# Optimization experiments

Measured on AMD Instinct MI355X. Metric: run time of the kernel, lower is better.

Reference implementation:

```python
import jax, jax.numpy as jnp
import numpy as np

DIM = 256
NUM_RFS = 256
OUT_DIM = 1024
N = 65536
M = 0.001


def setup_inputs() -> dict:
    key = jax.random.key(0)
    k1, k2, k3, k4, k5, k6 = jax.random.split(key, 6)
    x = jax.random.normal(k1, (N, DIM), dtype=jnp.float32)
    input_weights = jax.random.normal(k2, (OUT_DIM, DIM), dtype=jnp.float32)
    b = jax.random.normal(k3, (OUT_DIM,), dtype=jnp.float32)
    # projection matrix: normal(mean=0, std=0.02, size=(num_rfs, dim))
    proj = 0.02 * jax.random.normal(k4, (NUM_RFS, DIM), dtype=jnp.float32)
    # xis are complex points of the random-feature construction; keep small for exp stability
    xis_real = 0.1 * jax.random.normal(k5, (NUM_RFS,), dtype=jnp.float32)
    xis_imag = 0.1 * jax.random.normal(k6, (NUM_RFS,), dtype=jnp.float32)
    return {"x": x, "input_weights": input_weights, "b": b, "proj": proj,
            "xis_real": xis_real, "xis_imag": xis_imag}


def _asym_feats(xw, xis, proj, bias, is_weight):
    """create_asym_feats with a_fun/b_fun = identity, A_fun/B_fun = exp(xi*b).
    xw: (rows, DIM) float; xis: (NUM_RFS,) complex64; proj: (NUM_RFS, DIM) float.
    Returns (rows, NUM_RFS) complex64."""
    ab = xis  # ab_fun is identity -> ab_coeffs = xis
    scale = np.sqrt(1.0 + 4.0 * M).astype(np.float32)
    # renorm_gs[i] = sqrt(1+4M) * ab[i] * gs[i]  -> (NUM_RFS, DIM) complex
    renorm_gs = scale * ab[:, None] * proj.astype(jnp.complex64)
    # dot_products = xw_c @ renorm_gs.T  -> (rows, NUM_RFS) complex
    dot = jnp.einsum('nd,rd->nr', xw.astype(jnp.complex64), renorm_gs)
    sq = jnp.sum(xw * xw, axis=-1)  # (rows,)
    # correction: outer(sq/2, ab*ab) + M*||g_i||^2 (broadcast over rows)
    corr = (sq[:, None] * 0.5) * (ab * ab)[None, :]
    corr = corr + M * jnp.sum(proj * proj, axis=-1)[None, :]
    feats = jnp.exp(dot - corr) * np.float32(1.0 / np.sqrt(NUM_RFS))
    if is_weight:
        # AB_coeffs[j, i] = exp(xis[i] * bias[j])
        AB = jnp.exp(xis[None, :] * bias[:, None].astype(jnp.complex64))
        feats = AB * feats
    return feats


def reference(x, input_weights, b, proj, xis_real, xis_imag):
    xis = (xis_real + 1j * xis_imag).astype(jnp.complex64)
    # normalize=False path: scale weights and bias by dim**-0.25 at init time
    inv4 = np.float32(1.0 / DIM ** 0.25)
    w = input_weights * inv4
    bb = b * inv4
    c = np.float32((1.0 / np.sqrt(2.0)) * (1.0 + 4.0 * M) ** (DIM / 4.0))
    # precomputed weight features (parameter of the module)
    w_plus = _asym_feats(w, xis, proj, bb, is_weight=True)
    w_minus = _asym_feats(w, -xis, proj, bb, is_weight=True)
    weights = c * jnp.concatenate([w_plus, w_minus], axis=-1)  # (OUT_DIM, 2R) complex
    # forward: x scaled by 1/dim (normalize=False)
    xs = x * np.float32(1.0 / DIM)
    f_plus = _asym_feats(xs, xis, proj, bb, is_weight=False)
    f_minus = _asym_feats(xs, -xis, proj, bb, is_weight=False)
    feat = c * jnp.concatenate([f_plus, f_minus], axis=-1)  # (N, 2R) complex
    # (feat @ weights.T).real
    out = jnp.einsum('nr,or->no', feat, weights).real
    return out
```

## Files before the change

kernel.cpp:

```cpp
#include <hip/hip_runtime.h>
#include <cmath>
#include <cstdint>

#define NROWS 65536
#define DIMN  256
#define NRF   256
#define OUTD  1024
#define KDIM  1024
#define MCOEF 0.001f

typedef __bf16 v8bf __attribute__((ext_vector_type(8)));
typedef float  v4f  __attribute__((ext_vector_type(4)));
typedef unsigned short us8 __attribute__((ext_vector_type(8)));

__device__ __forceinline__ unsigned short f2bf(float f) {
  unsigned int u = __float_as_uint(f);
  u += 0x7fffu + ((u >> 16) & 1u);
  return (unsigned short)(u >> 16);
}

__device__ __forceinline__ void async_copy16(const void* g, void* l) {
  __builtin_amdgcn_global_load_lds(
      (const __attribute__((address_space(1))) void*)g,
      (__attribute__((address_space(3))) void*)l, 16, 0, 0);
}

__device__ __forceinline__ int sw_slot(int r, int c) {
  return r * 4 + ((c ^ (r >> 1)) & 3);
}

__global__ __launch_bounds__(64) void prep_rf(
    const float* __restrict__ proj, unsigned short* __restrict__ projbf,
    float* __restrict__ mg2) {
  int i = blockIdx.x;
  int lane = threadIdx.x;
  float4 v = ((const float4*)(proj + (size_t)i * DIMN))[lane];
  ushort4 o;
  o.x = f2bf(v.x); o.y = f2bf(v.y); o.z = f2bf(v.z); o.w = f2bf(v.w);
  ((ushort4*)(projbf + (size_t)i * DIMN))[lane] = o;
  float ss = v.x * v.x + v.y * v.y + v.z * v.z + v.w * v.w;
#pragma unroll
  for (int off = 32; off > 0; off >>= 1) ss += __shfl_down(ss, off, 64);
  if (lane == 0) mg2[i] = MCOEF * ss;
}

__global__ __launch_bounds__(256) void fused_features(
    const float* __restrict__ srcX,
    const float* __restrict__ srcW,
    const float* __restrict__ biasW,
    const float* __restrict__ xr_g, const float* __restrict__ xi_g,
    const float* __restrict__ mg2_g,
    const unsigned short* __restrict__ projbf,
    unsigned short* __restrict__ FX,
    unsigned short* __restrict__ FW,
    float sRx, float sRw, float scaleC) {
  __shared__ __align__(16) unsigned short big[16 * 1024];
  unsigned short* As = big;
  unsigned short* Bs = big + 2048;
  unsigned short* Os = big;
  __shared__ float xr_s[256], xi_s[256], c1_s[256], c2_s[256], mg2_s[256];
  __shared__ float sq_s[64], bias_s[64];

  int t = threadIdx.x;
  int lane = t & 63;
  int w = t >> 6;

  bool isW = blockIdx.x < (OUTD / 64);
  int blockRow = isW ? blockIdx.x * 64 : (blockIdx.x - OUTD / 64) * 64;
  const float* src = isW ? srcW : srcX;
  float scl = isW ? 0.25f : (1.f / DIMN);
  unsigned short* Fout = isW ? FW : FX;
  float sR = isW ? sRw : sRx;
  float sI = isW ? -sRw : sRx;

  {
    float a = xr_g[t], b = xi_g[t];
    xr_s[t] = a; xi_s[t] = b;
    c1_s[t] = a * a - b * b;
    c2_s[t] = 2.f * a * b;
    mg2_s[t] = mg2_g[t];
  }
  if (t < 64) bias_s[t] = isW ? biasW[blockRow + t] * 0.25f : 0.f;

  v4f acc[4][4];
#pragma unroll
  for (int a = 0; a < 4; a++)
#pragma unroll
    for (int b = 0; b < 4; b++)
#pragma unroll
      for (int q = 0; q < 4; q++) acc[a][b][q] = 0.f;

  int arow = t >> 2, sub = t & 3;
  const float* srow = src + (size_t)(blockRow + arow) * DIMN + sub * 8;
  float ss = 0.f;

  for (int kb = 0; kb < DIMN; kb += 32) {
    float4 v0 = *(const float4*)(srow + kb);
    float4 v1 = *(const float4*)(srow + kb + 4);
    v0.x *= scl; v0.y *= scl; v0.z *= scl; v0.w *= scl;
    v1.x *= scl; v1.y *= scl; v1.z *= scl; v1.w *= scl;
    ss += v0.x * v0.x + v0.y * v0.y + v0.z * v0.z + v0.w * v0.w +
          v1.x * v1.x + v1.y * v1.y + v1.z * v1.z + v1.w * v1.w;
    us8 o;
    o[0] = f2bf(v0.x); o[1] = f2bf(v0.y); o[2] = f2bf(v0.z); o[3] = f2bf(v0.w);
    o[4] = f2bf(v1.x); o[5] = f2bf(v1.y); o[6] = f2bf(v1.z); o[7] = f2bf(v1.w);
    *(us8*)&As[sw_slot(arow, sub) * 8] = o;
#pragma unroll
    for (int r = 0; r < 4; r++) {
      int idx = r * 256 + t;
      int row = idx >> 2, kc = ((idx & 3) ^ ((idx >> 3) & 3)) * 8;
      async_copy16(projbf + (size_t)row * DIMN + kb + kc,
                   Bs + (idx & ~63) * 8);
    }
    __syncthreads();
    v8bf af[4], bfv[4];
    int c = lane >> 4;
#pragma unroll
    for (int mi = 0; mi < 4; mi++)
      af[mi] = *(const v8bf*)&As[sw_slot(mi * 16 + (lane & 15), c) * 8];
#pragma unroll
    for (int ni = 0; ni < 4; ni++)
      bfv[ni] = *(const v8bf*)&Bs[sw_slot(w * 64 + ni * 16 + (lane & 15), c) * 8];
#pragma unroll
    for (int mi = 0; mi < 4; mi++)
#pragma unroll
      for (int ni = 0; ni < 4; ni++)
        acc[mi][ni] = __builtin_amdgcn_mfma_f32_16x16x32_bf16(
            af[mi], bfv[ni], acc[mi][ni], 0, 0, 0);
    __syncthreads();
  }

  ss += __shfl_xor(ss, 1, 64);
  ss += __shfl_xor(ss, 2, 64);
  if (sub == 0) sq_s[arow] = ss;

#pragma unroll
  for (int mi = 0; mi < 4; mi++) {
    __syncthreads();
#pragma unroll
    for (int ni = 0; ni < 4; ni++) {
      int i = w * 64 + ni * 16 + (lane & 15);
      float xrv = xr_s[i], xiv = xi_s[i];
      float c1v = c1_s[i], c2v = c2_s[i], mgv = mg2_s[i];
#pragma unroll
      for (int reg = 0; reg < 4; reg++) {
        int rl    = (lane >> 4) * 4 + reg;
        int rglob = mi * 16 + rl;
        float px = acc[mi][ni][reg];
        float tt = scaleC * px + bias_s[rglob];
        float u  = 0.5f * sq_s[rglob];
        float aa = u * c1v + mgv;
        float bb = u * c2v;
        float txr = tt * xrv;
        float txi = tt * xiv;
        float erp = __expf(txr - aa);
        float erm = __expf(-txr - aa);
        float s1, cc1, s2, cc2;
        __sincosf(txi - bb, &s1, &cc1);
        __sincosf(txi + bb, &s2, &cc2);
        ushort4 ov;
        ov.x = f2bf(sR * erp * cc1);
        ov.y = f2bf(sR * erm * cc2);
        ov.z = f2bf(sI * erp * s1);
        ov.w = f2bf(-sI * erm * s2);
        *(ushort4*)&Os[rl * KDIM + 4 * i] = ov;
      }
    }
    __syncthreads();
#pragma unroll
    for (int j = 0; j < 8; j++) {
      int chunk = j * 256 + t;
      int rowo  = chunk >> 7;
      int off   = (chunk & 127) * 8;
      *(us8*)(Fout + (size_t)(blockRow + mi * 16 + rowo) * KDIM + off) =
          *(const us8*)&Os[rowo * KDIM + off];
    }
  }
}

__global__ __launch_bounds__(256) void gemm_bt(
    const unsigned short* __restrict__ A,
    const unsigned short* __restrict__ B,
    float* __restrict__ C) {
  __shared__ __align__(16) unsigned short As[2][128 * 32];
  __shared__ __align__(16) unsigned short Bs[2][128 * 32];
  int t = threadIdx.x;
  int lane = t & 63;
  int w = t >> 6;
  int wm = w >> 1, wn = w & 1;
  int lid = blockIdx.x;
  int slot = lid >> 3;
  size_t bm = (size_t)(((lid & 7) * 64) + (slot >> 3)) * 128;
  size_t bn = (size_t)(slot & 7) * 128;

  v4f acc[4][4];
#pragma unroll
  for (int a = 0; a < 4; a++)
#pragma unroll
    for (int b = 0; b < 4; b++)
#pragma unroll
      for (int q = 0; q < 4; q++) acc[a][b][q] = 0.f;

  auto stage = [&](int buf, int kb) {
#pragma unroll
    for (int r = 0; r < 2; r++) {
      int idx = r * 256 + t;
      int row = idx >> 2, kc = ((idx & 3) ^ ((idx >> 3) & 3)) * 8;
      async_copy16(A + (bm + row) * KDIM + kb + kc, &As[buf][(idx & ~63) * 8]);
      async_copy16(B + (bn + row) * KDIM + kb + kc, &Bs[buf][(idx & ~63) * 8]);
    }
  };

  auto compute_tile = [&](int buf) {
    v8bf af[4], bfv[4];
    int c = lane >> 4;
#pragma unroll
    for (int mi = 0; mi < 4; mi++)
      af[mi] = *(const v8bf*)&As[buf][sw_slot(wm * 64 + mi * 16 + (lane & 15), c) * 8];
#pragma unroll
    for (int ni = 0; ni < 4; ni++)
      bfv[ni] = *(const v8bf*)&Bs[buf][sw_slot(wn * 64 + ni * 16 + (lane & 15), c) * 8];
#pragma unroll
    for (int mi = 0; mi < 4; mi++)
#pragma unroll
      for (int ni = 0; ni < 4; ni++)
        acc[mi][ni] = __builtin_amdgcn_mfma_f32_16x16x32_bf16(
            af[mi], bfv[ni], acc[mi][ni], 0, 0, 0);
  };

  stage(0, 0);
  asm volatile("s_waitcnt vmcnt(0)" ::: "memory");
  __syncthreads();
  int cur = 0;
  for (int kb = 32; kb < KDIM; kb += 32) {
    stage(cur ^ 1, kb);
    compute_tile(cur);
    asm volatile("s_waitcnt vmcnt(0)" ::: "memory");
    __syncthreads();
    cur ^= 1;
  }
  compute_tile(cur);

#pragma unroll
  for (int mi = 0; mi < 4; mi++)
#pragma unroll
    for (int ni = 0; ni < 4; ni++)
#pragma unroll
      for (int reg = 0; reg < 4; reg++) {
        size_t row = bm + wm * 64 + mi * 16 + (lane >> 4) * 4 + reg;
        size_t col = bn + wn * 64 + ni * 16 + (lane & 15);
        C[row * OUTD + col] = acc[mi][ni][reg];
      }
}

extern "C" void kernel_launch(void* const* d_in, const int* in_sizes, int n_in,
                              void* d_out, int out_size, void* d_ws, size_t ws_size,
                              hipStream_t stream) {
  (void)in_sizes; (void)n_in; (void)out_size;
  const float* x    = (const float*)d_in[0];
  const float* iw   = (const float*)d_in[1];
  const float* bvec = (const float*)d_in[2];
  const float* proj = (const float*)d_in[3];
  const float* xr   = (const float*)d_in[4];
  const float* xi   = (const float*)d_in[5];
  float* out = (float*)d_out;

  char* ws = (char*)d_ws;
  size_t off = 0;
  auto take = [&](size_t bytes) {
    char* p = ws + off;
    off = (off + bytes + 255) & ~(size_t)255;
    return p;
  };
  unsigned short* F      = (unsigned short*)take((size_t)NROWS * KDIM * 2);
  unsigned short* Wp     = (unsigned short*)take((size_t)OUTD * KDIM * 2);
  unsigned short* projbf = (unsigned short*)take((size_t)NRF * DIMN * 2);
  float* mg2 = (float*)take((size_t)NRF * 4);
  if (ws_size < off) return;

  const float  scaleC = sqrtf(1.f + 4.f * MCOEF);
  const double c2d    = 0.5 * exp(128.0 * log(1.0 + 4.0 * 0.001));
  const float  invSR  = 0.0625f;
  const float  sRw    = (float)(c2d * 0.0625);

  prep_rf<<<NRF, 64, 0, stream>>>(proj, projbf, mg2);
  fused_features<<<NROWS / 64 + OUTD / 64, 256, 0, stream>>>(
      x, iw, bvec, xr, xi, mg2, projbf, F, Wp, invSR, sRw, scaleC);
  gemm_bt<<<4096, 256, 0, stream>>>(F, Wp, out);
}
```

Baseline: 516.2 us.

## Rewrite GEMM as 256x256 tile, 8-wave kernel with quarter-staged async prefetch

Replaces the 128x128x32 two-buffer GEMM with a 256x256x64 tile run by 512 threads (8 waves), cutting the grid from 4096 to 1024 blocks. Each k-step is split into four quadrant MFMA phases, and the next tile's half-tile loads are interleaved between them with partial vmcnt waits and setprio, so LDS reads, global loads and matrix math overlap. The block-to-tile mapping is remapped so neighbouring blocks share data. The larger tiles raise reuse of A and B and lower global traffic, at the cost of 128 KB of LDS per block, many accumulator registers, one block per CU and more barriers per step.

```diff
diff --git a/kernel.cpp b/kernel.cpp
--- a/kernel.cpp
+++ b/kernel.cpp
@@ -178,79 +178,142 @@
   }
 }
 
-__global__ __launch_bounds__(256) void gemm_bt(
+#define WAITV(N) asm volatile("s_waitcnt vmcnt(" #N ")" ::: "memory")
+
+__global__ __launch_bounds__(512) void gemm_bt(
     const unsigned short* __restrict__ A,
     const unsigned short* __restrict__ B,
     float* __restrict__ C) {
-  __shared__ __align__(16) unsigned short As[2][128 * 32];
-  __shared__ __align__(16) unsigned short Bs[2][128 * 32];
-  int t = threadIdx.x;
-  int lane = t & 63;
-  int w = t >> 6;
-  int wm = w >> 1, wn = w & 1;
+  __shared__ __align__(16) unsigned short As[2][256 * 64];
+  __shared__ __align__(16) unsigned short Bs[2][256 * 64];
+  int tt = threadIdx.x;
+  int lane = tt & 63;
+  int wv = tt >> 6;
+  int wm = wv >> 2, wn = wv & 3;
+
   int lid = blockIdx.x;
-  int slot = lid >> 3;
-  size_t bm = (size_t)(((lid & 7) * 64) + (slot >> 3)) * 128;
-  size_t bn = (size_t)(slot & 7) * 128;
-
-  v4f acc[4][4];
-#pragma unroll
-  for (int a = 0; a < 4; a++)
+  int wg = (lid & 7) * 128 + (lid >> 3);
+  size_t bm = (size_t)(wg >> 2) * 256;
+  size_t bn = (size_t)(wg & 3) * 256;
+
+  unsigned int offA[2][2], offB[2][2];
+#pragma unroll
+  for (int h = 0; h < 2; h++)
+#pragma unroll
+    for (int i = 0; i < 2; i++) {
+      int L = i * 512 + tt;
+      int rho = h * 128 + (L >> 3);
+      int c = (L & 7) ^ (rho & 7);
+      int gA = ((rho >> 6) & 1) * 128 + (rho >> 7) * 64 + (rho & 63);
+      int gB = ((rho >> 5) & 3) * 64 + (rho >> 7) * 32 + (rho & 31);
+      offA[h][i] = (unsigned int)((bm + gA) * KDIM + c * 8);
+      offB[h][i] = (unsigned int)((bn + gB) * KDIM + c * 8);
+    }
+
+#define STAGE_A(H, KB) do { \
+  _Pragma("unroll") for (int i_ = 0; i_ < 2; i_++) \
+    async_copy16(A + offA[H][i_] + (KB), \
+                 &As[nbuf][((H) * 1024 + i_ * 512 + (tt & ~63)) * 8]); \
+} while (0)
+#define STAGE_B(H, KB) do { \
+  _Pragma("unroll") for (int i_ = 0; i_ < 2; i_++) \
+    async_copy16(B + offB[H][i_] + (KB), \
+                 &Bs[nbuf][((H) * 1024 + i_ * 512 + (tt & ~63)) * 8]); \
+} while (0)
+
+  v8bf af[4][2], b0[2][2], b1[2][2];
+  v4f acc[8][4];
+#pragma unroll
+  for (int a = 0; a < 8; a++)
 #pragma unroll
     for (int b = 0; b < 4; b++)
 #pragma unroll
       for (int q = 0; q < 4; q++) acc[a][b][q] = 0.f;
 
-  auto stage = [&](int buf, int kb) {
-#pragma unroll
-    for (int r = 0; r < 2; r++) {
-      int idx = r * 256 + t;
-      int row = idx >> 2, kc = ((idx & 3) ^ ((idx >> 3) & 3)) * 8;
-      async_copy16(A + (bm + row) * KDIM + kb + kc, &As[buf][(idx & ~63) * 8]);
-      async_copy16(B + (bn + row) * KDIM + kb + kc, &Bs[buf][(idx & ~63) * 8]);
-    }
-  };
-
-  auto compute_tile = [&](int buf) {
-    v8bf af[4], bfv[4];
-    int c = lane >> 4;
-#pragma unroll
-    for (int mi = 0; mi < 4; mi++)
-      af[mi] = *(const v8bf*)&As[buf][sw_slot(wm * 64 + mi * 16 + (lane & 15), c) * 8];
-#pragma unroll
-    for (int ni = 0; ni < 4; ni++)
-      bfv[ni] = *(const v8bf*)&Bs[buf][sw_slot(wn * 64 + ni * 16 + (lane & 15), c) * 8];
-#pragma unroll
-    for (int mi = 0; mi < 4; mi++)
-#pragma unroll
-      for (int ni = 0; ni < 4; ni++)
-        acc[mi][ni] = __builtin_amdgcn_mfma_f32_16x16x32_bf16(
-            af[mi], bfv[ni], acc[mi][ni], 0, 0, 0);
-  };
-
-  stage(0, 0);
-  asm volatile("s_waitcnt vmcnt(0)" ::: "memory");
-  __syncthreads();
-  int cur = 0;
-  for (int kb = 32; kb < KDIM; kb += 32) {
-    stage(cur ^ 1, kb);
-    compute_tile(cur);
-    asm volatile("s_waitcnt vmcnt(0)" ::: "memory");
-    __syncthreads();
-    cur ^= 1;
-  }
-  compute_tile(cur);
-
-#pragma unroll
-  for (int mi = 0; mi < 4; mi++)
-#pragma unroll
-    for (int ni = 0; ni < 4; ni++)
+#define READ_A(MH) do { \
+  _Pragma("unroll") for (int mf_ = 0; mf_ < 4; mf_++) { \
+    int rho_ = (MH) * 128 + wm * 64 + mf_ * 16 + (lane & 15); \
+    int sw_ = rho_ & 7; \
+    const unsigned short* rp_ = &As[buf][rho_ * 64]; \
+    af[mf_][0] = *(const v8bf*)&rp_[(((lane >> 4)) ^ sw_) * 8]; \
+    af[mf_][1] = *(const v8bf*)&rp_[((4 + (lane >> 4)) ^ sw_) * 8]; \
+  } \
+} while (0)
+#define READ_B(NH, DST) do { \
+  _Pragma("unroll") for (int nf_ = 0; nf_ < 2; nf_++) { \
+    int rho_ = (NH) * 128 + wn * 32 + nf_ * 16 + (lane & 15); \
+    int sw_ = rho_ & 7; \
+    const unsigned short* rp_ = &Bs[buf][rho_ * 64]; \
+    DST[nf_][0] = *(const v8bf*)&rp_[(((lane >> 4)) ^ sw_) * 8]; \
+    DST[nf_][1] = *(const v8bf*)&rp_[((4 + (lane >> 4)) ^ sw_) * 8]; \
+  } \
+} while (0)
+#define MMA_Q(MH, NH, BSRC) do { \
+  __builtin_amdgcn_s_setprio(1); \
+  _Pragma("unroll") for (int mf_ = 0; mf_ < 4; mf_++) \
+  _Pragma("unroll") for (int nf_ = 0; nf_ < 2; nf_++) \
+  _Pragma("unroll") for (int ks_ = 0; ks_ < 2; ks_++) \
+    acc[(MH) * 4 + mf_][(NH) * 2 + nf_] = \
+        __builtin_amdgcn_mfma_f32_16x16x32_bf16( \
+            af[mf_][ks_], BSRC[nf_][ks_], \
+            acc[(MH) * 4 + mf_][(NH) * 2 + nf_], 0, 0, 0); \
+  __builtin_amdgcn_s_setprio(0); \
+} while (0)
+
+  {
+    const int nbuf = 0;
+    STAGE_A(0, 0); STAGE_B(0, 0); STAGE_B(1, 0); STAGE_A(1, 0);
+  }
+  WAITV(4);
+  __builtin_amdgcn_s_barrier();
+
+  for (int t = 0; t < 16; ++t) {
+    const int buf = t & 1, nbuf = buf ^ 1;
+    const bool pf = (t < 15);
+    const int kb = (t + 1) * 64;
+
+    READ_A(0); READ_B(0, b0);
+    if (pf) STAGE_A(0, kb);
+    __builtin_amdgcn_s_barrier();
+    MMA_Q(0, 0, b0);
+    if (pf) { WAITV(4); } else { WAITV(2); }
+    __builtin_amdgcn_s_barrier();
+
+    READ_B(1, b1);
+    if (pf) STAGE_B(0, kb);
+    __builtin_amdgcn_s_barrier();
+    MMA_Q(0, 1, b1);
+    if (pf) { WAITV(4); } else { WAITV(0); }
+    __builtin_amdgcn_s_barrier();
+
+    READ_A(1);
+    if (pf) STAGE_B(1, kb);
+    __builtin_amdgcn_s_barrier();
+    MMA_Q(1, 1, b1);
+    __builtin_amdgcn_s_barrier();
+
+    if (pf) STAGE_A(1, kb);
+    __builtin_amdgcn_s_barrier();
+    MMA_Q(1, 0, b0);
+    if (pf) { WAITV(4); }
+    __builtin_amdgcn_s_barrier();
+  }
+
+#pragma unroll
+  for (int mf = 0; mf < 8; mf++)
+#pragma unroll
+    for (int nf = 0; nf < 4; nf++)
 #pragma unroll
       for (int reg = 0; reg < 4; reg++) {
-        size_t row = bm + wm * 64 + mi * 16 + (lane >> 4) * 4 + reg;
-        size_t col = bn + wn * 64 + ni * 16 + (lane & 15);
-        C[row * OUTD + col] = acc[mi][ni][reg];
+        size_t row = bm + wm * 128 + mf * 16 + (lane >> 4) * 4 + reg;
+        size_t col = bn + wn * 64 + nf * 16 + (lane & 15);
+        C[row * OUTD + col] = acc[mf][nf][reg];
       }
+#undef STAGE_A
+#undef STAGE_B
+#undef READ_A
+#undef READ_B
+#undef MMA_Q
 }
 
 extern "C" void kernel_launch(void* const* d_in, const int* in_sizes, int n_in,
@@ -286,5 +349,5 @@
   prep_rf<<<NRF, 64, 0, stream>>>(proj, projbf, mg2);
   fused_features<<<NROWS / 64 + OUTD / 64, 256, 0, stream>>>(
       x, iw, bvec, xr, xi, mg2, projbf, F, Wp, invSR, sRw, scaleC);
-  gemm_bt<<<4096, 256, 0, stream>>>(F, Wp, out);
-}
+  gemm_bt<<<1024, 512, 0, stream>>>(F, Wp, out);
+}
```

Result: no change. 506.8 us (-1.8%).
